# Kernel optimization log

Hardware: AMD Instinct MI355X
Metric: run time of the kernel (lower is better)

Reference implementation:

```python
import jax, jax.numpy as jnp
import numpy as np

B, S, D = 4, 2048, 1024
H = 16
DH = D // H


def setup_inputs() -> dict:
    key = jax.random.key(0)
    ks = jax.random.split(key, 5)
    scale = 1.0 / np.sqrt(D)
    return {
        "x": jax.random.normal(ks[0], (B, S, D), dtype=jnp.float32),
        "wq": jax.random.normal(ks[1], (D, D), dtype=jnp.float32) * scale,
        "wk": jax.random.normal(ks[2], (D, D), dtype=jnp.float32) * scale,
        "wv": jax.random.normal(ks[3], (D, D), dtype=jnp.float32) * scale,
        "wo": jax.random.normal(ks[4], (D, D), dtype=jnp.float32) * scale,
    }


def reference(x, wq, wk, wv, wo):
    b, s, d = x.shape
    # nn.Linear applies x @ W.T (weights are [out, in])
    q = (x @ wq.T).reshape(b, s, H, DH).transpose(0, 2, 1, 3)  # [b,h,s,dh]
    k = (x @ wk.T).reshape(b, s, H, DH).transpose(0, 2, 1, 3)
    v = (x @ wv.T).reshape(b, s, H, DH).transpose(0, 2, 1, 3)
    scale = 1.0 / jnp.sqrt(jnp.asarray(DH, dtype=x.dtype))
    scores = jnp.einsum("bhqd,bhkd->bhqk", q, k) * scale  # [b,h,s,s]
    causal = jnp.tril(jnp.ones((s, s), dtype=bool))
    scores = jnp.where(causal, scores, -jnp.inf)
    attn = jax.nn.softmax(scores, axis=-1)
    out = jnp.einsum("bhqk,bhkd->bhqd", attn, v)  # [b,h,s,dh]
    out = out.transpose(0, 2, 1, 3).reshape(b, s, d)
    return out @ wo.T
```

## Files before the change

### kernel.cpp

```cpp
#include <hip/hip_runtime.h>
#include <hip/hip_bf16.h>

#define Bz 4
#define Sz 2048
#define Dz 1024
#define Hz 16
#define DHz 64

typedef __bf16 bf16x8 __attribute__((ext_vector_type(8)));
typedef float f32x4 __attribute__((ext_vector_type(4)));
typedef short s16x4 __attribute__((ext_vector_type(4)));
typedef unsigned short u16x4 __attribute__((ext_vector_type(4)));

#define SCQF 0.18033688011112042f

__global__ __launch_bounds__(256) void cvt_f32_bf16(const float* __restrict__ src,
                                                    __hip_bfloat16* __restrict__ dst, int n) {
    int i = (blockIdx.x * 256 + threadIdx.x) * 4;
    if (i >= n) return;
    float4 f = *reinterpret_cast<const float4*>(src + i);
    dst[i + 0] = __float2bfloat16(f.x);
    dst[i + 1] = __float2bfloat16(f.y);
    dst[i + 2] = __float2bfloat16(f.z);
    dst[i + 3] = __float2bfloat16(f.w);
}

__global__ __launch_bounds__(256) void cvt_w4(const float* __restrict__ w0, const float* __restrict__ w1,
                                              const float* __restrict__ w2, const float* __restrict__ w3,
                                              __hip_bfloat16* __restrict__ dst) {
    constexpr int WEL = Dz * Dz;
    int i = (blockIdx.x * 256 + threadIdx.x) * 4;
    const int which = i >> 20;
    const float* src = (which == 0) ? w0 : (which == 1) ? w1 : (which == 2) ? w2 : w3;
    float4 f = *reinterpret_cast<const float4*>(src + (i & (WEL - 1)));
    dst[i + 0] = __float2bfloat16(f.x);
    dst[i + 1] = __float2bfloat16(f.y);
    dst[i + 2] = __float2bfloat16(f.z);
    dst[i + 3] = __float2bfloat16(f.w);
}

__device__ __forceinline__ void gl2lds16(const __hip_bfloat16* g, __hip_bfloat16* l) {
    __builtin_amdgcn_global_load_lds(
        (const __attribute__((address_space(1))) void*)g,
        (__attribute__((address_space(3))) void*)l, 16, 0, 0);
}

__device__ __forceinline__ unsigned ldsaddr(const void* p) {
    return (unsigned)(size_t)(const __attribute__((address_space(3))) void*)p;
}

template <int N, int K, typename OT, int MODE, bool SCQ = false>
__device__ __forceinline__ void gemm128_body(const __hip_bfloat16* __restrict__ A,
                                             const __hip_bfloat16* __restrict__ W,
                                             OT* __restrict__ C, int bm, int bn,
                                             __hip_bfloat16* As, __hip_bfloat16* Bs) {
    const int tid  = threadIdx.x;
    const int wid  = tid >> 6;
    const int lane = tid & 63;
    const int quad = lane >> 4;
    const int l16  = lane & 15;
    const int wr = wid >> 1, wc = wid & 1;

    const int srow = wid * 32 + (lane >> 2);
    const int scol = (lane & 3) * 8;
    const __hip_bfloat16* gA = A + (size_t)(bm * 128 + srow) * K + scol;
    const __hip_bfloat16* gB = W + (size_t)(bn * 128 + srow) * K + scol;
    __hip_bfloat16* lA = &As[(wid * 32) * 32];
    __hip_bfloat16* lB = &Bs[(wid * 32) * 32];

    f32x4 acc[4][4] = {};

    for (int k0 = 0; k0 < K; k0 += 32) {
        __syncthreads();
        gl2lds16(gA + k0,                  lA);
        gl2lds16(gA + (size_t)16 * K + k0, lA + 16 * 32);
        gl2lds16(gB + k0,                  lB);
        gl2lds16(gB + (size_t)16 * K + k0, lB + 16 * 32);
        __syncthreads();

        bf16x8 af[4], bf[4];
#pragma unroll
        for (int mi = 0; mi < 4; ++mi)
            af[mi] = *reinterpret_cast<const bf16x8*>(&As[(wr * 64 + mi * 16 + l16) * 32 + quad * 8]);
#pragma unroll
        for (int ni = 0; ni < 4; ++ni)
            bf[ni] = *reinterpret_cast<const bf16x8*>(&Bs[(wc * 64 + ni * 16 + l16) * 32 + quad * 8]);
#pragma unroll
        for (int mi = 0; mi < 4; ++mi)
#pragma unroll
            for (int ni = 0; ni < 4; ++ni)
                acc[mi][ni] = __builtin_amdgcn_mfma_f32_16x16x32_bf16(af[mi], bf[ni], acc[mi][ni], 0, 0, 0);
    }

#pragma unroll
    for (int mi = 0; mi < 4; ++mi)
#pragma unroll
        for (int ni = 0; ni < 4; ++ni) {
            const int row0 = bm * 128 + wr * 64 + mi * 16 + quad * 4;
            const int col  = bn * 128 + wc * 64 + ni * 16 + l16;
#pragma unroll
            for (int r = 0; r < 4; ++r) {
                const int row = row0 + r;
                float v = acc[mi][ni][r];
                if constexpr (SCQ) v *= SCQF;
                if constexpr (MODE == 0) {
                    if constexpr (__is_same(OT, float))
                        C[(size_t)row * N + col] = v;
                    else
                        C[(size_t)row * N + col] = __float2bfloat16(v);
                } else if constexpr (MODE == 1) {
                    const int bh = (row >> 11) * Hz + (col >> 6);
                    C[(size_t)bh * (Sz * DHz) + (size_t)(row & 2047) * 64 + (col & 63)] =
                        __float2bfloat16(v);
                } else {
                    const int bh = (row >> 11) * Hz + (col >> 6);
                    C[(size_t)bh * (Sz * DHz) + (size_t)((col >> 4) & 3) * (Sz * 16) +
                      (size_t)(row & 2047) * 16 + (col & 15)] = __float2bfloat16(v);
                }
            }
        }
}

template <int M, int N, int K, typename OT>
__global__ __launch_bounds__(256) void gemm128(const __hip_bfloat16* __restrict__ A,
                                               const __hip_bfloat16* __restrict__ W,
                                               OT* __restrict__ C) {
    __shared__ __hip_bfloat16 As[128 * 32];
    __shared__ __hip_bfloat16 Bs[128 * 32];
    constexpr int NB = N / 128;
    gemm128_body<N, K, OT, 0>(A, W, C, blockIdx.x / NB, blockIdx.x % NB, As, Bs);
}

template <int M, int K>
__global__ __launch_bounds__(256) void gemm_qkv(const __hip_bfloat16* __restrict__ A,
                                                const __hip_bfloat16* __restrict__ W0,
                                                const __hip_bfloat16* __restrict__ W1,
                                                const __hip_bfloat16* __restrict__ W2,
                                                __hip_bfloat16* __restrict__ C0,
                                                __hip_bfloat16* __restrict__ C1,
                                                __hip_bfloat16* __restrict__ C2) {
    __shared__ __hip_bfloat16 As[128 * 32];
    __shared__ __hip_bfloat16 Bs[128 * 32];
    constexpr int NB = Dz / 128;
    const int which = blockIdx.x % 3;
    const int rem   = blockIdx.x / 3;
    const int bm = rem / NB, bn = rem % NB;
    if (which == 0)      gemm128_body<Dz, K, __hip_bfloat16, 0, true>(A, W0, C0, bm, bn, As, Bs);
    else if (which == 1) gemm128_body<Dz, K, __hip_bfloat16, 1>(A, W1, C1, bm, bn, As, Bs);
    else                 gemm128_body<Dz, K, __hip_bfloat16, 2>(A, W2, C2, bm, bn, As, Bs);
}

__device__ __forceinline__ f32x4 mfma16bf(s16x4 a, s16x4 b, f32x4 c) {
#if __has_builtin(__builtin_amdgcn_mfma_f32_16x16x16bf16_1k)
    return __builtin_amdgcn_mfma_f32_16x16x16bf16_1k(a, b, c, 0, 0, 0);
#else
    asm volatile("v_mfma_f32_16x16x16_bf16 %0, %1, %2, %0" : "+v"(c) : "v"(a), "v"(b));
    return c;
#endif
}

#define TRD(i, off) \
    asm volatile("ds_read_b64_tr_b16 %0, %1 offset:" off : "=v"(vf[i]) : "v"(va))

__global__ __launch_bounds__(256, 4) void attn_mfma7(const __hip_bfloat16* __restrict__ Q,
                                                     const __hip_bfloat16* __restrict__ Kh,
                                                     const __hip_bfloat16* __restrict__ Vh,
                                                     __hip_bfloat16* __restrict__ O) {
    __shared__ __hip_bfloat16 Ks[2][64 * 64];
    __shared__ __hip_bfloat16 Vs[2][64 * 64];

    const int tid  = threadIdx.x;
    const int wid  = tid >> 6;
    const int lane = tid & 63;
    const int quad = lane >> 4;
    const int l16  = lane & 15;

    const int xcd  = blockIdx.x & 7;
    const int j    = blockIdx.x >> 3;
    const int bh   = xcd * 8 + (j >> 4);
    const int pair = j & 15;
    const int h    = bh & 15;
    const int b    = bh >> 4;
    const size_t baseQ = (size_t)b * Sz * Dz + (size_t)h * DHz;
    const size_t kvb   = (size_t)bh * (Sz * DHz);

    const int rlo = lane >> 3;
    const int xel = ((lane & 7) ^ rlo) * 8;

    auto stage = [&](int kn, int bf_) {
#pragma unroll
        for (int c = 0; c < 2; ++c) {
            gl2lds16(Kh + kvb + (size_t)(kn + wid * 16 + c * 8 + rlo) * 64 + xel,
                     &Ks[bf_][(wid * 16 + c * 8) * 64]);
            gl2lds16(Vh + kvb + (size_t)wid * (Sz * 16) + (size_t)(kn + c * 32 + (lane >> 1)) * 16 + (lane & 1) * 8,
                     &Vs[bf_][wid * 1024 + c * 512]);
        }
    };

    const unsigned vb0 = ldsaddr(&Vs[0][0]) + lane * 8;
    const unsigned sw  = (l16 & 7) << 4;

    const s16x4 ones = {(short)0x3F80, (short)0x3F80, (short)0x3F80, (short)0x3F80};

    int buf = 0;
    stage(0, 0);
    __syncthreads();

#pragma unroll 1
    for (int p = 0; p < 2; ++p) {
        const int qblk  = (p == 0) ? pair : 31 - pair;
        const int q0    = qblk * 64 + wid * 16;
        const int niter = qblk + 1;

        const __hip_bfloat16* qp = Q + baseQ + (size_t)(q0 + l16) * Dz + quad * 8;
        const bf16x8 qf0 = *reinterpret_cast<const bf16x8*>(qp);
        const bf16x8 qf1 = *reinterpret_cast<const bf16x8*>(qp + 32);

        float m = -1e30f;
        f32x4 ot[4] = {};
        f32x4 lacc  = {};

#pragma unroll 1
        for (int it = 0; it < niter; ++it) {
            const int k0 = it * 64;

            f32x4 st[4] = {};
            {
                const char* Kp = (const char*)&Ks[buf][0];
#pragma unroll
                for (int s = 0; s < 4; ++s) {
                    const int rb = (s * 16 + l16) * 128;
                    const bf16x8 a0 = *reinterpret_cast<const bf16x8*>(Kp + rb + ((quad * 16) ^ sw));
                    const bf16x8 a1 = *reinterpret_cast<const bf16x8*>(Kp + rb + ((quad * 16 + 64) ^ sw));
                    st[s] = __builtin_amdgcn_mfma_f32_16x16x32_bf16(a0, qf0, st[s], 0, 0, 0);
                    st[s] = __builtin_amdgcn_mfma_f32_16x16x32_bf16(a1, qf1, st[s], 0, 0, 0);
                }
            }

            const bool more = (it + 1 < niter);
            if (more)        stage(k0 + 64, buf ^ 1);
            else if (p == 0) stage(0,       buf ^ 1);

            float sv[16];
            if (it == niter - 1) {
                const int qrow = q0 + l16;
#pragma unroll
                for (int s = 0; s < 4; ++s)
#pragma unroll
                    for (int r = 0; r < 4; ++r) {
                        const int key = k0 + s * 16 + quad * 4 + r;
                        sv[s * 4 + r] = (key <= qrow) ? st[s][r] : -1e30f;
                    }
            } else {
#pragma unroll
                for (int s = 0; s < 4; ++s)
#pragma unroll
                    for (int r = 0; r < 4; ++r) sv[s * 4 + r] = st[s][r];
            }

            const float p0 = fmaxf(fmaxf(sv[0],  sv[1]),  sv[2]);
            const float p1 = fmaxf(fmaxf(sv[3],  sv[4]),  sv[5]);
            const float p2 = fmaxf(fmaxf(sv[6],  sv[7]),  sv[8]);
            const float p3 = fmaxf(fmaxf(sv[9],  sv[10]), sv[11]);
            const float p4 = fmaxf(fmaxf(sv[12], sv[13]), sv[14]);
            const float p5 = fmaxf(fmaxf(p0, p1), p2);
            float tmax = fmaxf(fmaxf(fmaxf(p5, p3), p4), sv[15]);
            tmax = fmaxf(tmax, __shfl_xor(tmax, 16, 64));
            tmax = fmaxf(tmax, __shfl_xor(tmax, 32, 64));

            const float mnew = fmaxf(m, tmax);
            const bool  skip = __all(tmax <= m);
            if (!skip) {
                const float alpha = __builtin_amdgcn_exp2f(m - mnew);
                m = mnew;
#pragma unroll
                for (int s = 0; s < 4; ++s) ot[s] *= alpha;
                lacc[0] *= alpha;
            }

            float pv[16];
#pragma unroll
            for (int i = 0; i < 16; ++i) pv[i] = __builtin_amdgcn_exp2f(sv[i] - m);

            s16x4 vf[16];
            const unsigned va = vb0 + (unsigned)(buf << 13);
            TRD(0, "0");    TRD(1, "512");  TRD(2, "1024"); TRD(3, "1536");
            TRD(4, "2048"); TRD(5, "2560"); TRD(6, "3072"); TRD(7, "3584");

            s16x4 pw[4];
#pragma unroll
            for (int s = 0; s < 4; ++s)
#pragma unroll
                for (int r = 0; r < 4; ++r) {
                    union { __hip_bfloat16 hh; short uu; } cv;
                    cv.hh = __float2bfloat16(pv[s * 4 + r]);
                    pw[s][r] = cv.uu;
                }

            lacc = mfma16bf(ones, pw[0], lacc);
            lacc = mfma16bf(ones, pw[1], lacc);
            lacc = mfma16bf(ones, pw[2], lacc);
            lacc = mfma16bf(ones, pw[3], lacc);

            asm volatile("s_waitcnt lgkmcnt(0)" ::: "memory");
            __builtin_amdgcn_sched_barrier(0);
            TRD(8,  "4096"); TRD(9,  "4608"); TRD(10, "5120"); TRD(11, "5632");
            TRD(12, "6144"); TRD(13, "6656"); TRD(14, "7168"); TRD(15, "7680");

            ot[0] = mfma16bf(vf[0],  pw[0], ot[0]);
            ot[0] = mfma16bf(vf[1],  pw[1], ot[0]);
            ot[0] = mfma16bf(vf[2],  pw[2], ot[0]);
            ot[0] = mfma16bf(vf[3],  pw[3], ot[0]);
            ot[1] = mfma16bf(vf[4],  pw[0], ot[1]);
            ot[1] = mfma16bf(vf[5],  pw[1], ot[1]);
            ot[1] = mfma16bf(vf[6],  pw[2], ot[1]);
            ot[1] = mfma16bf(vf[7],  pw[3], ot[1]);

            asm volatile("s_waitcnt lgkmcnt(0)" ::: "memory");
            __builtin_amdgcn_sched_barrier(0);
            ot[2] = mfma16bf(vf[8],  pw[0], ot[2]);
            ot[2] = mfma16bf(vf[9],  pw[1], ot[2]);
            ot[2] = mfma16bf(vf[10], pw[2], ot[2]);
            ot[2] = mfma16bf(vf[11], pw[3], ot[2]);
            ot[3] = mfma16bf(vf[12], pw[0], ot[3]);
            ot[3] = mfma16bf(vf[13], pw[1], ot[3]);
            ot[3] = mfma16bf(vf[14], pw[2], ot[3]);
            ot[3] = mfma16bf(vf[15], pw[3], ot[3]);

            __syncthreads();
            buf ^= 1;
        }

        const float linv = 1.f / lacc[0];
        __hip_bfloat16* op = O + baseQ + (size_t)(q0 + l16) * Dz + quad * 4;
#pragma unroll
        for (int sd = 0; sd < 4; ++sd) {
            u16x4 w;
#pragma unroll
            for (int r = 0; r < 4; ++r) {
                union { __hip_bfloat16 hh; unsigned short uu; } cv;
                cv.hh = __float2bfloat16(ot[sd][r] * linv);
                w[r] = cv.uu;
            }
            *reinterpret_cast<u16x4*>(op + sd * 16) = w;
        }
    }
}

extern "C" void kernel_launch(void* const* d_in, const int* in_sizes, int n_in,
                              void* d_out, int out_size, void* d_ws, size_t ws_size,
                              hipStream_t stream) {
    const float* x  = (const float*)d_in[0];
    const float* wq = (const float*)d_in[1];
    const float* wk = (const float*)d_in[2];
    const float* wv = (const float*)d_in[3];
    const float* wo = (const float*)d_in[4];
    float* out = (float*)d_out;

    constexpr int TOK = Bz * Sz * Dz;
    constexpr int WEL = Dz * Dz;

    __hip_bfloat16* xb  = (__hip_bfloat16*)d_ws;
    __hip_bfloat16* wqb = xb  + TOK;
    __hip_bfloat16* wkb = wqb + WEL;
    __hip_bfloat16* wvb = wkb + WEL;
    __hip_bfloat16* wob = wvb + WEL;
    __hip_bfloat16* Qb  = wob + WEL;
    __hip_bfloat16* Kh  = Qb + TOK;
    __hip_bfloat16* Vh  = (__hip_bfloat16*)d_out;
    __hip_bfloat16* Ob  = xb;

    cvt_f32_bf16<<<TOK / 4 / 256, 256, 0, stream>>>(x, xb, TOK);
    cvt_w4<<<4 * WEL / 4 / 256, 256, 0, stream>>>(wq, wk, wv, wo, wqb);

    constexpr int M = Bz * Sz;
    constexpr int GB = (M / 128) * (Dz / 128);

    gemm_qkv<M, Dz><<<3 * GB, 256, 0, stream>>>(xb, wqb, wkb, wvb, Qb, Kh, Vh);

    const int ATTN_BLOCKS = Bz * Hz * 16;
    attn_mfma7<<<ATTN_BLOCKS, 256, 0, stream>>>(Qb, Kh, Vh, Ob);

    gemm128<M, Dz, Dz, float><<<GB, 256, 0, stream>>>(Ob, wob, out);
}
```

Measured before the change: 247.4 us.

## Double GEMM K-tile to 64 with XOR-swizzled LDS and fuse conversion kernels

The GEMM main loop now stages 64-wide K tiles per barrier pair instead of 32, halving the number of sync/load rounds. LDS rows are XOR-swizzled on both the global-to-LDS writes and the fragment reads to avoid bank conflicts. The two fp32→bf16 conversion launches are merged into a single kernel over x and all four weights. In exchange LDS use per block doubles, which may reduce occupancy.

```diff
diff --git a/kernel.cpp b/kernel.cpp
--- a/kernel.cpp
+++ b/kernel.cpp
@@ -14,25 +14,23 @@
 
 #define SCQF 0.18033688011112042f
 
-__global__ __launch_bounds__(256) void cvt_f32_bf16(const float* __restrict__ src,
-                                                    __hip_bfloat16* __restrict__ dst, int n) {
-    int i = (blockIdx.x * 256 + threadIdx.x) * 4;
-    if (i >= n) return;
-    float4 f = *reinterpret_cast<const float4*>(src + i);
-    dst[i + 0] = __float2bfloat16(f.x);
-    dst[i + 1] = __float2bfloat16(f.y);
-    dst[i + 2] = __float2bfloat16(f.z);
-    dst[i + 3] = __float2bfloat16(f.w);
-}
-
-__global__ __launch_bounds__(256) void cvt_w4(const float* __restrict__ w0, const float* __restrict__ w1,
-                                              const float* __restrict__ w2, const float* __restrict__ w3,
-                                              __hip_bfloat16* __restrict__ dst) {
+__global__ __launch_bounds__(256) void cvt_all(const float* __restrict__ x,
+                                               const float* __restrict__ w0, const float* __restrict__ w1,
+                                               const float* __restrict__ w2, const float* __restrict__ w3,
+                                               __hip_bfloat16* __restrict__ dst) {
+    constexpr int TOK = Bz * Sz * Dz;
     constexpr int WEL = Dz * Dz;
     int i = (blockIdx.x * 256 + threadIdx.x) * 4;
-    const int which = i >> 20;
-    const float* src = (which == 0) ? w0 : (which == 1) ? w1 : (which == 2) ? w2 : w3;
-    float4 f = *reinterpret_cast<const float4*>(src + (i & (WEL - 1)));
+    const float* src;
+    if (i < TOK) {
+        src = x + i;
+    } else {
+        const int jj = i - TOK;
+        const int which = jj >> 20;
+        const float* w = (which == 0) ? w0 : (which == 1) ? w1 : (which == 2) ? w2 : w3;
+        src = w + (jj & (WEL - 1));
+    }
+    float4 f = *reinterpret_cast<const float4*>(src);
     dst[i + 0] = __float2bfloat16(f.x);
     dst[i + 1] = __float2bfloat16(f.y);
     dst[i + 2] = __float2bfloat16(f.z);
@@ -61,35 +59,45 @@
     const int l16  = lane & 15;
     const int wr = wid >> 1, wc = wid & 1;
 
-    const int srow = wid * 32 + (lane >> 2);
-    const int scol = (lane & 3) * 8;
-    const __hip_bfloat16* gA = A + (size_t)(bm * 128 + srow) * K + scol;
-    const __hip_bfloat16* gB = W + (size_t)(bn * 128 + srow) * K + scol;
-    __hip_bfloat16* lA = &As[(wid * 32) * 32];
-    __hip_bfloat16* lB = &Bs[(wid * 32) * 32];
+    const int rlo = lane >> 3;
+    const int xel = ((lane & 7) ^ rlo) * 8;
+    const __hip_bfloat16* gA = A + (size_t)(bm * 128 + wid * 32 + rlo) * K + xel;
+    const __hip_bfloat16* gB = W + (size_t)(bn * 128 + wid * 32 + rlo) * K + xel;
+    __hip_bfloat16* lA = &As[(wid * 32) * 64];
+    __hip_bfloat16* lB = &Bs[(wid * 32) * 64];
+
+    const unsigned sw = (unsigned)((l16 & 7) << 4);
+    const char* Ap = (const char*)As;
+    const char* Bp = (const char*)Bs;
 
     f32x4 acc[4][4] = {};
 
-    for (int k0 = 0; k0 < K; k0 += 32) {
+    for (int k0 = 0; k0 < K; k0 += 64) {
         __syncthreads();
-        gl2lds16(gA + k0,                  lA);
-        gl2lds16(gA + (size_t)16 * K + k0, lA + 16 * 32);
-        gl2lds16(gB + k0,                  lB);
-        gl2lds16(gB + (size_t)16 * K + k0, lB + 16 * 32);
+#pragma unroll
+        for (int c = 0; c < 4; ++c) {
+            gl2lds16(gA + (size_t)(c * 8) * K + k0, lA + (c * 8) * 64);
+            gl2lds16(gB + (size_t)(c * 8) * K + k0, lB + (c * 8) * 64);
+        }
         __syncthreads();
 
-        bf16x8 af[4], bf[4];
-#pragma unroll
-        for (int mi = 0; mi < 4; ++mi)
-            af[mi] = *reinterpret_cast<const bf16x8*>(&As[(wr * 64 + mi * 16 + l16) * 32 + quad * 8]);
-#pragma unroll
-        for (int ni = 0; ni < 4; ++ni)
-            bf[ni] = *reinterpret_cast<const bf16x8*>(&Bs[(wc * 64 + ni * 16 + l16) * 32 + quad * 8]);
-#pragma unroll
-        for (int mi = 0; mi < 4; ++mi)
+#pragma unroll
+        for (int kk = 0; kk < 2; ++kk) {
+            bf16x8 af[4], bf[4];
+#pragma unroll
+            for (int mi = 0; mi < 4; ++mi)
+                af[mi] = *reinterpret_cast<const bf16x8*>(
+                    Ap + (wr * 64 + mi * 16 + l16) * 128 + ((kk * 64 + quad * 16) ^ sw));
 #pragma unroll
             for (int ni = 0; ni < 4; ++ni)
-                acc[mi][ni] = __builtin_amdgcn_mfma_f32_16x16x32_bf16(af[mi], bf[ni], acc[mi][ni], 0, 0, 0);
+                bf[ni] = *reinterpret_cast<const bf16x8*>(
+                    Bp + (wc * 64 + ni * 16 + l16) * 128 + ((kk * 64 + quad * 16) ^ sw));
+#pragma unroll
+            for (int mi = 0; mi < 4; ++mi)
+#pragma unroll
+                for (int ni = 0; ni < 4; ++ni)
+                    acc[mi][ni] = __builtin_amdgcn_mfma_f32_16x16x32_bf16(af[mi], bf[ni], acc[mi][ni], 0, 0, 0);
+        }
     }
 
 #pragma unroll
@@ -125,8 +133,8 @@
 __global__ __launch_bounds__(256) void gemm128(const __hip_bfloat16* __restrict__ A,
                                                const __hip_bfloat16* __restrict__ W,
                                                OT* __restrict__ C) {
-    __shared__ __hip_bfloat16 As[128 * 32];
-    __shared__ __hip_bfloat16 Bs[128 * 32];
+    __shared__ __hip_bfloat16 As[128 * 64];
+    __shared__ __hip_bfloat16 Bs[128 * 64];
     constexpr int NB = N / 128;
     gemm128_body<N, K, OT, 0>(A, W, C, blockIdx.x / NB, blockIdx.x % NB, As, Bs);
 }
@@ -139,8 +147,8 @@
                                                 __hip_bfloat16* __restrict__ C0,
                                                 __hip_bfloat16* __restrict__ C1,
                                                 __hip_bfloat16* __restrict__ C2) {
-    __shared__ __hip_bfloat16 As[128 * 32];
-    __shared__ __hip_bfloat16 Bs[128 * 32];
+    __shared__ __hip_bfloat16 As[128 * 64];
+    __shared__ __hip_bfloat16 Bs[128 * 64];
     constexpr int NB = Dz / 128;
     const int which = blockIdx.x % 3;
     const int rem   = blockIdx.x / 3;
@@ -370,8 +378,7 @@
     __hip_bfloat16* Vh  = (__hip_bfloat16*)d_out;
     __hip_bfloat16* Ob  = xb;
 
-    cvt_f32_bf16<<<TOK / 4 / 256, 256, 0, stream>>>(x, xb, TOK);
-    cvt_w4<<<4 * WEL / 4 / 256, 256, 0, stream>>>(wq, wk, wv, wo, wqb);
+    cvt_all<<<(TOK + 4 * WEL) / 4 / 256, 256, 0, stream>>>(x, wq, wk, wv, wo, xb);
 
     constexpr int M = Bz * Sz;
     constexpr int GB = (M / 128) * (Dz / 128);
```

Measured after the change: 237.2 us. 1.04x faster.
